# Optimization experiments

Hardware: AMD Instinct MI355X
Metric: run time of the kernel (lower is better)

The kernel has to match this reference:

```python
import jax, jax.numpy as jnp
import numpy as np

N, S, D = 8, 448, 768
VS, DS = 50000, 256
VP, DP = 200, 128
VM, DM = 400, 128
VA, DA = 360, 128
EPS_LS = 0.1
LN_EPS = 1e-12
SQRT2 = 1.4142135623730951


def setup_inputs() -> dict:
    key = jax.random.key(0)
    ks = jax.random.split(key, 20)
    total = N * S
    # all sequence lengths == S; next-token prediction uses tokens [0, S-2] as
    # inputs (hidden_sel) and tokens [1, S-1] as targets (target_sel)
    hidden_sel = np.concatenate([i * S + np.arange(S - 1) for i in range(N)]).astype(np.int32)
    target_sel = np.concatenate([i * S + np.arange(1, S) for i in range(N)]).astype(np.int32)
    tokens_lengths = (np.arange(total) % 4).astype(np.int32)  # per-token affix counts
    affix_sel = np.nonzero(tokens_lengths[target_sel] > 0)[0].astype(np.int32)

    def p(k, shape):
        return jax.random.normal(k, shape, jnp.float32) * 0.02

    inp = {
        "tr_hidden_state": jax.random.normal(ks[0], (S, N, D), jnp.float32),
        "affixes_prob": jax.random.uniform(ks[1], (total, VA), dtype=jnp.float32),
        "stems": jax.random.randint(ks[2], (total,), 0, VS, jnp.int32),
        "pos_tags": jax.random.randint(ks[3], (total,), 0, VP, jnp.int32),
        "lm_morphs": jax.random.randint(ks[4], (total,), 0, VM, jnp.int32),
        "hidden_sel_idx": jnp.asarray(hidden_sel),
        "target_sel_idx": jnp.asarray(target_sel),
        "affix_sel_idx": jnp.asarray(affix_sel),
        # stem head
        "stem_emb": p(ks[5], (VS, DS)), "stem_W": p(ks[6], (D, DS)),
        "stem_b": jnp.zeros((DS,)), "stem_g": jnp.ones((DS,)),
        "stem_beta": jnp.zeros((DS,)), "stem_bias": jnp.zeros((VS,)),
        # pos-tag head
        "pos_emb": p(ks[7], (VP, DP)), "pos_W": p(ks[8], (D, DP)),
        "pos_b": jnp.zeros((DP,)), "pos_g": jnp.ones((DP,)),
        "pos_beta": jnp.zeros((DP,)), "pos_bias": jnp.zeros((VP,)),
        # lm-morph head
        "morph_emb": p(ks[9], (VM, DM)), "morph_W": p(ks[10], (D, DM)),
        "morph_b": jnp.zeros((DM,)), "morph_g": jnp.ones((DM,)),
        "morph_beta": jnp.zeros((DM,)), "morph_bias": jnp.zeros((VM,)),
        # affixes head
        "aff_emb": p(ks[11], (VA, DA)), "aff_W": p(ks[12], (D, DA)),
        "aff_b": jnp.zeros((DA,)), "aff_g": jnp.ones((DA,)),
        "aff_beta": jnp.zeros((DA,)), "aff_bias": jnp.zeros((VA,)),
    }
    return inp


def _gelu(x):
    return x * 0.5 * (1.0 + jax.lax.erf(x / SQRT2))


def _ln(x, g, b):
    m = x.mean(-1, keepdims=True)
    v = ((x - m) ** 2).mean(-1, keepdims=True)
    return (x - m) * jax.lax.rsqrt(v + LN_EPS) * g + b


def _head(x, W, b, g, beta, emb, bias):
    h = _ln(_gelu(x @ W + b), g, beta)  # BaseHeadTransform
    return h @ emb.T + bias             # tied decoder + bias


def _ls_nll(lprobs, tgt):
    # label_smoothed_nll_loss with reduce=True, no ignore_index
    nll = -jnp.take_along_axis(lprobs, tgt[:, None], axis=1)[:, 0]
    smooth = -lprobs.sum(-1)
    nll_m, sm_m = nll.mean(), smooth.mean()
    eps_i = EPS_LS / (lprobs.shape[-1] - 1)
    return (1.0 - EPS_LS - eps_i) * nll_m + eps_i * sm_m, nll_m


def reference(tr_hidden_state, affixes_prob, stems, pos_tags, lm_morphs,
              hidden_sel_idx, target_sel_idx, affix_sel_idx,
              stem_emb, stem_W, stem_b, stem_g, stem_beta, stem_bias,
              pos_emb, pos_W, pos_b, pos_g, pos_beta, pos_bias,
              morph_emb, morph_W, morph_b, morph_g, morph_beta, morph_bias,
              aff_emb, aff_W, aff_b, aff_g, aff_beta, aff_bias):
    flat = jnp.transpose(tr_hidden_state, (1, 0, 2)).reshape(N * S, D)
    x = flat[hidden_sel_idx]  # [T, D] ragged gather of predictor states

    stem_lp = jax.nn.log_softmax(_head(x, stem_W, stem_b, stem_g, stem_beta, stem_emb, stem_bias), axis=-1)
    stem_loss, stem_nll = _ls_nll(stem_lp, stems[target_sel_idx])

    pos_lp = jax.nn.log_softmax(_head(x, pos_W, pos_b, pos_g, pos_beta, pos_emb, pos_bias), axis=-1)
    pos_loss, pos_nll = _ls_nll(pos_lp, pos_tags[target_sel_idx])

    morph_lp = jax.nn.log_softmax(_head(x, morph_W, morph_b, morph_g, morph_beta, morph_emb, morph_bias), axis=-1)
    morph_loss, morph_nll = _ls_nll(morph_lp, lm_morphs[target_sel_idx])

    xa = x[affix_sel_idx]                                # tokens with affixes
    ta = affixes_prob[target_sel_idx][affix_sel_idx]     # [Ta, VA]
    z = _head(xa, aff_W, aff_b, aff_g, aff_beta, aff_emb, aff_bias)
    aff_loss = jnp.mean(jnp.maximum(z, 0.0) - z * ta + jnp.log1p(jnp.exp(-jnp.abs(z))))

    return jnp.stack([stem_loss, pos_loss, morph_loss, aff_loss, stem_nll, pos_nll, morph_nll])
```

## Files before the change

kernel.cpp:

```cpp
#include <hip/hip_runtime.h>
#include <cstdint>
#include <cstddef>


typedef __attribute__((ext_vector_type(8))) __bf16 bf16x8;
typedef __attribute__((ext_vector_type(4))) float f32x4;
typedef __attribute__((ext_vector_type(4))) unsigned short u16x4;
typedef __attribute__((ext_vector_type(2))) unsigned short u16x2;

namespace {
constexpr int S_LEN   = 448;
constexpr int N_SEQ   = 8;
constexpr int D_MODEL = 768;
constexpr int TPAD    = 3584;
constexpr int VS = 50000, VP = 200, VM = 400, VA = 360;
constexpr int DS_STEM = 256, DS_POS = 128, DS_MORPH = 128, DS_AFF = 128;
constexpr int VS_PAD = 50176;
constexpr int VCHUNK = 32;
constexpr int VITERS = 3136 / VCHUNK;
constexpr float PAD_E = (float)(VS_PAD - VS);
constexpr int NVB_P = 1;
constexpr int NVB_M = 2;
}

__device__ __forceinline__ unsigned short f2bf(float f) {
  unsigned int u = __float_as_uint(f);
  unsigned int r = (u + 0x7FFFu + ((u >> 16) & 1u)) >> 16;
  return (unsigned short)r;
}
__device__ __forceinline__ float bf2f(unsigned short u) {
  return __uint_as_float(((unsigned int)u) << 16);
}


__global__ __launch_bounds__(256) void gather_x_kernel(
    const float* __restrict__ tr, const int* __restrict__ hsel,
    const int* __restrict__ tsel, const int* __restrict__ asel,
    const int* __restrict__ stems, const int* __restrict__ postags,
    const int* __restrict__ morphs,
    unsigned short* __restrict__ x, int* __restrict__ tgtS, int* __restrict__ tgtP,
    int* __restrict__ tgtM, int* __restrict__ arow, int T, int Ta) {
  const size_t e = (size_t)blockIdx.x * 256 + threadIdx.x;
  const int t = (int)(e / D_MODEL);
  const int d = (int)(e % D_MODEL);
  float v = 0.f;
  if (t < T) {
    int idx = hsel[t];
    int n = idx / S_LEN, s = idx % S_LEN;
    v = tr[((size_t)s * N_SEQ + n) * D_MODEL + d];
  }
  x[e] = f2bf(v);
  if (e < (size_t)T) {
    int tt = tsel[e];
    tgtS[e] = stems[tt]; tgtP[e] = postags[tt]; tgtM[e] = morphs[tt];
  }
  if (e < (size_t)Ta) arow[e] = tsel[asel[e]];
}

__global__ __launch_bounds__(256) void transpose_all_kernel(
    const float* __restrict__ sW, const float* __restrict__ pW,
    const float* __restrict__ mW, const float* __restrict__ aW,
    unsigned short* __restrict__ wtS, unsigned short* __restrict__ wtP,
    unsigned short* __restrict__ wtM, unsigned short* __restrict__ wtA) {
  const int e = blockIdx.x * 256 + threadIdx.x;
  const float* W; unsigned short* Wt; int DS; int local;
  if (e < 196608)      { W = sW; Wt = wtS; DS = 256; local = e; }
  else if (e < 294912) { W = pW; Wt = wtP; DS = 128; local = e - 196608; }
  else if (e < 393216) { W = mW; Wt = wtM; DS = 128; local = e - 294912; }
  else                 { W = aW; Wt = wtA; DS = 128; local = e - 393216; }
  const int n = local / D_MODEL, k = local % D_MODEL;
  Wt[local] = f2bf(W[(size_t)k * DS + n]);
}

__global__ __launch_bounds__(256) void conv_emb_all_kernel(
    const float* __restrict__ sE, const float* __restrict__ pE,
    const float* __restrict__ mE, const float* __restrict__ aE,
    const float* __restrict__ sb,
    unsigned short* __restrict__ dS, unsigned short* __restrict__ dP,
    unsigned short* __restrict__ dM, unsigned short* __restrict__ dA,
    float* __restrict__ bp) {
  const size_t q = ((size_t)blockIdx.x * 256 + threadIdx.x) * 4;
  if (q >= 13008896) {
    const size_t local = q - 13008896;
    float4 v = make_float4(0.f, 0.f, 0.f, 0.f);
    if (local < (size_t)VS) v = *(const float4*)(sb + local);
    *(float4*)(bp + local) = v;
    return;
  }
  const float* src; unsigned short* dst; size_t local, real;
  if (q < 12845056)            { src = sE; dst = dS; local = q;            real = 12800000; }
  else if (q < 12877824)       { src = pE; dst = dP; local = q - 12845056; real = 25600; }
  else if (q < 12943360)       { src = mE; dst = dM; local = q - 12877824; real = 51200; }
  else                         { src = aE; dst = dA; local = q - 12943360; real = 46080; }
  float4 v = make_float4(0.f, 0.f, 0.f, 0.f);
  if (local < real) v = *(const float4*)(src + local);
  u16x4 o = { f2bf(v.x), f2bf(v.y), f2bf(v.z), f2bf(v.w) };
  *(u16x4*)(dst + local) = o;
}

template <int NT>
__device__ __forceinline__ void head_body(
    const unsigned short* __restrict__ x, const unsigned short* __restrict__ Wt,
    const float* __restrict__ bvec, const float* __restrict__ gvec,
    const float* __restrict__ betav, unsigned short* __restrict__ hout) {
  constexpr int DS = NT * 16;
  const int lane = threadIdx.x & 63;
  const int wave = threadIdx.x >> 6;
  const int row0 = blockIdx.x * 32 + wave * 16;
  const int lrow = lane & 15;
  const int lk8  = (lane >> 4) * 8;

  f32x4 acc[NT];
#pragma unroll
  for (int nt = 0; nt < NT; ++nt) acc[nt] = f32x4{0.f, 0.f, 0.f, 0.f};

  const unsigned short* xrow = x + (size_t)(row0 + lrow) * D_MODEL + lk8;
#pragma unroll
  for (int ks = 0; ks < 24; ++ks) {
    bf16x8 a = *(const bf16x8*)(xrow + ks * 32);
#pragma unroll
    for (int nt = 0; nt < NT; ++nt) {
      bf16x8 b = *(const bf16x8*)(Wt + (size_t)(nt * 16 + lrow) * D_MODEL + ks * 32 + lk8);
      acc[nt] = __builtin_amdgcn_mfma_f32_16x16x32_bf16(a, b, acc[nt], 0, 0, 0);
    }
  }

  float bb[NT], gg[NT], be[NT];
#pragma unroll
  for (int nt = 0; nt < NT; ++nt) {
    int c = nt * 16 + lrow;
    bb[nt] = bvec[c]; gg[nt] = gvec[c]; be[nt] = betav[c];
  }
#pragma unroll
  for (int r = 0; r < 4; ++r) {
    const int row = row0 + (lane >> 4) * 4 + r;
    float vals[NT];
    float s = 0.f, s2 = 0.f;
#pragma unroll
    for (int nt = 0; nt < NT; ++nt) {
      float v = acc[nt][r] + bb[nt];
      v = 0.5f * v * (1.f + erff(v * 0.70710678118654752f));
      vals[nt] = v; s += v; s2 += v * v;
    }
    s  += __shfl_xor(s, 1);  s  += __shfl_xor(s, 2);  s  += __shfl_xor(s, 4);  s  += __shfl_xor(s, 8);
    s2 += __shfl_xor(s2, 1); s2 += __shfl_xor(s2, 2); s2 += __shfl_xor(s2, 4); s2 += __shfl_xor(s2, 8);
    const float mean = s * (1.f / DS);
    const float var  = s2 * (1.f / DS) - mean * mean;
    const float rstd = rsqrtf(var + 1e-12f);
#pragma unroll
    for (int nt = 0; nt < NT; ++nt) {
      float o = (vals[nt] - mean) * rstd * gg[nt] + be[nt];
      hout[(size_t)row * DS + nt * 16 + lrow] = f2bf(o);
    }
  }
}

__global__ __launch_bounds__(128, 2) void head_all_kernel(
    const unsigned short* __restrict__ x,
    const unsigned short* __restrict__ wtS, const float* __restrict__ sb,
    const float* __restrict__ sg, const float* __restrict__ sbe, unsigned short* __restrict__ hS,
    const unsigned short* __restrict__ wtP, const float* __restrict__ pb,
    const float* __restrict__ pg, const float* __restrict__ pbe, unsigned short* __restrict__ hP,
    const unsigned short* __restrict__ wtM, const float* __restrict__ mb,
    const float* __restrict__ mg, const float* __restrict__ mbe, unsigned short* __restrict__ hM,
    const unsigned short* __restrict__ wtA, const float* __restrict__ ab,
    const float* __restrict__ ag, const float* __restrict__ abe, unsigned short* __restrict__ hA) {
  if (blockIdx.y == 3)      head_body<16>(x, wtS, sb, sg, sbe, hS);
  else if (blockIdx.y == 0) head_body<8>(x, wtP, pb, pg, pbe, hP);
  else if (blockIdx.y == 1) head_body<8>(x, wtM, mb, mg, mbe, hM);
  else                      head_body<8>(x, wtA, ab, ag, abe, hA);
}


__device__ __forceinline__ void stem_role(
    const unsigned short* __restrict__ h, const unsigned short* __restrict__ emb,
    const float* __restrict__ bpad, float* __restrict__ psum,
    float* __restrict__ psum2, char* smem) {
  unsigned short (*lbuf)[4096] = (unsigned short(*)[4096])smem;
  float* lbias = (float*)(smem + 32768);

  const int f   = blockIdx.x;
  const int k2  = f >> 3;
  const int bx  = k2 % 7;
  const int by  = (k2 / 7) * 8 + (f & 7);
  const int tid  = threadIdx.x;
  const int lane = tid & 63;
  const int wave = tid >> 6;
  const int lrow = lane & 15;
  const int hi   = lane >> 4;
  const int lk8  = hi * 8;
  const int tok0 = bx * 512 + wave * 64;
  const int vbase0 = by * (VITERS * 16);

  for (int i = tid; i < VITERS * 16; i += 512) lbias[i] = bpad[vbase0 + i];

  bf16x8 hB[4][8];
#pragma unroll
  for (int tt = 0; tt < 4; ++tt)
#pragma unroll
    for (int ks = 0; ks < 8; ++ks)
      hB[tt][ks] = *(const bf16x8*)(h + (size_t)(tok0 + tt * 16 + lrow) * 256 + ks * 32 + lk8);

  const int dst16 = tid * 16;
  const int srow  = dst16 >> 9;
  const int sbyte = dst16 ^ ((srow & 7) << 4);
  const char* gs  = (const char*)emb + (size_t)vbase0 * 512 + sbyte;

  auto stage = [&](int buf, int it) {
    __builtin_amdgcn_global_load_lds(
        (const __attribute__((address_space(1))) unsigned int*)(gs + (size_t)it * 8192),
        (__attribute__((address_space(3))) unsigned int*)(&lbuf[buf][wave * 512]),
        16, 0, 0);
  };

  int loff[8];
#pragma unroll
  for (int ks = 0; ks < 8; ++ks)
    loff[ks] = (lrow * 512 + ks * 64 + hi * 16) ^ ((lrow & 7) << 4);

  float esum[4] = {0.f, 0.f, 0.f, 0.f};
  float ssum[4] = {0.f, 0.f, 0.f, 0.f};

  stage(0, 0); stage(1, 1); stage(2, 2);
  __syncthreads();

#pragma unroll 1
  for (int it = 0; it < VITERS; ++it) {
    if (it <= VITERS - 3)      asm volatile("s_waitcnt vmcnt(2)" ::: "memory");
    else if (it == VITERS - 2) asm volatile("s_waitcnt vmcnt(1)" ::: "memory");
    else                       asm volatile("s_waitcnt vmcnt(0)" ::: "memory");
    __builtin_amdgcn_s_barrier();
    if (it + 3 < VITERS) stage((it + 3) & 3, it + 3);

    const float4 bv = *(const float4*)(lbias + it * 16 + hi * 4);
    const char* lp = (const char*)(&lbuf[it & 3][0]);
    bf16x8 aA[8];
#pragma unroll
    for (int ks = 0; ks < 8; ++ks)
      aA[ks] = *(const bf16x8*)(lp + loff[ks]);

#pragma unroll
    for (int tt = 0; tt < 4; ++tt) {
      f32x4 acc = f32x4{0.f, 0.f, 0.f, 0.f};
#pragma unroll
      for (int ks = 0; ks < 8; ++ks)
        acc = __builtin_amdgcn_mfma_f32_16x16x32_bf16(aA[ks], hB[tt][ks], acc, 0, 0, 0);
      const float v0 = acc[0] + bv.x, v1 = acc[1] + bv.y;
      const float v2 = acc[2] + bv.z, v3 = acc[3] + bv.w;
      esum[tt] += (__expf(v0) + __expf(v1)) + (__expf(v2) + __expf(v3));
      ssum[tt] += (v0 + v1) + (v2 + v3);
    }
  }

#pragma unroll
  for (int tt = 0; tt < 4; ++tt) {
    float e = esum[tt], s = ssum[tt];
    e += __shfl_xor(e, 16); e += __shfl_xor(e, 32);
    s += __shfl_xor(s, 16); s += __shfl_xor(s, 32);
    if (hi == 0) {
      const int tok = tok0 + tt * 16 + lrow;
      psum [(size_t)tok * VCHUNK + by] = e;
      psum2[(size_t)tok * VCHUNK + by] = s;
    }
  }
}

__device__ __forceinline__ void pm_role(
    const unsigned short* __restrict__ h, const unsigned short* __restrict__ emb,
    const float* __restrict__ bias, float* __restrict__ psum,
    float* __restrict__ psum2, int V, int NVB, int vbx, int vby, char* smem) {
  const int t256 = threadIdx.x & 255;
  const int w8   = threadIdx.x >> 6;
  const int grp  = threadIdx.x >> 8;
  const int lane = t256 & 63;
  const int wave4 = t256 >> 6;
  const int colbase = vby * 256 + wave4 * 64;
  const int row0 = vbx * 32;
  const int lrow = lane & 15;
  const int hi   = lane >> 4;
  const int lk8  = hi * 8;
  float (*lds_e)[32] = (float(*)[32])smem;
  float (*lds_s)[32] = (float(*)[32])(smem + 1024);

  bf16x8 bfr[4][4];
  float bv[4];
  bool mk[4];
#pragma unroll
  for (int nt = 0; nt < 4; ++nt) {
    int col = colbase + nt * 16 + lrow;
#pragma unroll
    for (int ks = 0; ks < 4; ++ks)
      bfr[ks][nt] = *(const bf16x8*)(emb + (size_t)col * 128 + ks * 32 + lk8);
    mk[nt] = (col < V);
    bv[nt] = mk[nt] ? bias[col] : 0.f;
  }

  f32x4 acc[2][4];
#pragma unroll
  for (int rt = 0; rt < 2; ++rt)
#pragma unroll
    for (int nt = 0; nt < 4; ++nt) acc[rt][nt] = f32x4{0.f, 0.f, 0.f, 0.f};

  const unsigned short* hrow = h + (size_t)(row0 + lrow) * 128 + lk8;
#pragma unroll
  for (int ks = 0; ks < 4; ++ks) {
#pragma unroll
    for (int rt = 0; rt < 2; ++rt) {
      bf16x8 a = *(const bf16x8*)(hrow + (size_t)rt * 16 * 128 + ks * 32);
#pragma unroll
      for (int nt = 0; nt < 4; ++nt)
        acc[rt][nt] = __builtin_amdgcn_mfma_f32_16x16x32_bf16(a, bfr[ks][nt], acc[rt][nt], 0, 0, 0);
    }
  }

#pragma unroll
  for (int rt = 0; rt < 2; ++rt)
#pragma unroll
    for (int r = 0; r < 4; ++r) {
      float e = 0.f, s = 0.f;
#pragma unroll
      for (int nt = 0; nt < 4; ++nt) {
        float v = acc[rt][nt][r] + bv[nt];
        float ev = __expf(v);
        e += mk[nt] ? ev : 0.f;
        s += mk[nt] ? v : 0.f;
      }
      e += __shfl_xor(e, 1); e += __shfl_xor(e, 2); e += __shfl_xor(e, 4); e += __shfl_xor(e, 8);
      s += __shfl_xor(s, 1); s += __shfl_xor(s, 2); s += __shfl_xor(s, 4); s += __shfl_xor(s, 8);
      if (lrow == 0) {
        lds_e[w8][rt * 16 + hi * 4 + r] = e;
        lds_s[w8][rt * 16 + hi * 4 + r] = s;
      }
    }
  __syncthreads();
  if (t256 < 32) {
    const int rr = t256;
    const int b4 = grp * 4;
    float e = lds_e[b4][rr] + lds_e[b4 + 1][rr] + lds_e[b4 + 2][rr] + lds_e[b4 + 3][rr];
    float s = lds_s[b4][rr] + lds_s[b4 + 1][rr] + lds_s[b4 + 2][rr] + lds_s[b4 + 3][rr];
    const int row = row0 + rr;
    psum [(size_t)row * NVB + vby] = e;
    psum2[(size_t)row * NVB + vby] = s;
  }
}

__device__ __forceinline__ void aff_role(
    const unsigned short* __restrict__ h, const unsigned short* __restrict__ emb,
    const float* __restrict__ bias, const int* __restrict__ asel,
    const int* __restrict__ arow, const float* __restrict__ aprob,
    float* __restrict__ partial, int Ta, int gaff, int bx, char* smem) {
  const int t256 = threadIdx.x & 255;
  const int grp  = threadIdx.x >> 8;
  const int w8   = threadIdx.x >> 6;
  const int lane = t256 & 63;
  const int wave4 = t256 >> 6;
  const int colbase = grp * 256 + wave4 * 64;
  const int lrow = lane & 15;
  const int lk8  = (lane >> 4) * 8;
  float* wred = (float*)smem;

  bf16x8 bfr[4][4];
  float bv[4];
  bool mk[4];
#pragma unroll
  for (int nt = 0; nt < 4; ++nt) {
    int col = colbase + nt * 16 + lrow;
#pragma unroll
    for (int ks = 0; ks < 4; ++ks)
      bfr[ks][nt] = *(const bf16x8*)(emb + (size_t)col * DS_AFF + ks * 32 + lk8);
    mk[nt] = (col < VA);
    bv[nt] = mk[nt] ? bias[col] : 0.f;
  }

  float lsum = 0.f;
  {
    const int rb = bx * 16;
    const int ia = rb + lrow;
    const int srow = (ia < Ta) ? asel[ia] : 0;
    f32x4 acc[4];
#pragma unroll
    for (int nt = 0; nt < 4; ++nt) acc[nt] = f32x4{0.f, 0.f, 0.f, 0.f};
    const unsigned short* hrow = h + (size_t)srow * DS_AFF + lk8;
#pragma unroll
    for (int ks = 0; ks < 4; ++ks) {
      bf16x8 a = *(const bf16x8*)(hrow + ks * 32);
#pragma unroll
      for (int nt = 0; nt < 4; ++nt)
        acc[nt] = __builtin_amdgcn_mfma_f32_16x16x32_bf16(a, bfr[ks][nt], acc[nt], 0, 0, 0);
    }
#pragma unroll
    for (int r = 0; r < 4; ++r) {
      const int i2 = rb + (lane >> 4) * 4 + r;
      const bool live = (i2 < Ta);
      const int trow = live ? arow[i2] : 0;
#pragma unroll
      for (int nt = 0; nt < 4; ++nt) {
        if (live && mk[nt]) {
          float z = acc[nt][r] + bv[nt];
          float ta = aprob[(size_t)trow * VA + (colbase + nt * 16 + lrow)];
          lsum += fmaxf(z, 0.f) - z * ta + log1pf(__expf(-fabsf(z)));
        }
      }
    }
  }
#pragma unroll
  for (int m = 1; m < 64; m <<= 1) lsum += __shfl_xor(lsum, m);
  if (lane == 0) wred[w8] = lsum;
  __syncthreads();
  if (t256 == 0) {
    const int b4 = grp * 4;
    partial[grp * gaff + bx] = wred[b4] + wred[b4 + 1] + wred[b4 + 2] + wred[b4 + 3];
  }
}

__device__ __forceinline__ void tgt_role(
    const unsigned short* __restrict__ hS, const unsigned short* __restrict__ embS,
    const float* __restrict__ bS, const int* __restrict__ tgtS_,
    const unsigned short* __restrict__ hP, const unsigned short* __restrict__ embP,
    const float* __restrict__ bP, const int* __restrict__ tgtP_,
    const unsigned short* __restrict__ hM, const unsigned short* __restrict__ embM,
    const float* __restrict__ bM, const int* __restrict__ tgtM_,
    float* __restrict__ tlog, int T, int vb) {
  const int lane = threadIdx.x & 63;
  const int wave = threadIdx.x >> 6;
  const int t = vb * 8 + wave;
  if (t >= T) return;
  const int tg = tgtS_[t], tp = tgtP_[t], tm = tgtM_[t];
  u16x4 hv = *(const u16x4*)(hS + (size_t)t * 256 + lane * 4);
  u16x4 ev = *(const u16x4*)(embS + (size_t)tg * 256 + lane * 4);
  float d0 = bf2f(hv[0]) * bf2f(ev[0]) + bf2f(hv[1]) * bf2f(ev[1]) +
             bf2f(hv[2]) * bf2f(ev[2]) + bf2f(hv[3]) * bf2f(ev[3]);
  u16x2 hp = *(const u16x2*)(hP + (size_t)t * 128 + lane * 2);
  u16x2 ep = *(const u16x2*)(embP + (size_t)tp * 128 + lane * 2);
  float d1 = bf2f(hp[0]) * bf2f(ep[0]) + bf2f(hp[1]) * bf2f(ep[1]);
  u16x2 hm = *(const u16x2*)(hM + (size_t)t * 128 + lane * 2);
  u16x2 em = *(const u16x2*)(embM + (size_t)tm * 128 + lane * 2);
  float d2 = bf2f(hm[0]) * bf2f(em[0]) + bf2f(hm[1]) * bf2f(em[1]);
#pragma unroll
  for (int m = 1; m < 64; m <<= 1) {
    d0 += __shfl_xor(d0, m); d1 += __shfl_xor(d1, m); d2 += __shfl_xor(d2, m);
  }
  if (lane == 0) {
    tlog[t]            = d0 + bS[tg];
    tlog[TPAD + t]     = d1 + bP[tp];
    tlog[2 * TPAD + t] = d2 + bM[tm];
  }
}

__global__ __launch_bounds__(512, 2) void mega_stats_kernel(
    const unsigned short* __restrict__ hS, const unsigned short* __restrict__ embS,
    const float* __restrict__ bpadS, float* __restrict__ psS, float* __restrict__ ps2S,
    const unsigned short* __restrict__ hP, const unsigned short* __restrict__ embP,
    const float* __restrict__ p_bias, float* __restrict__ psP, float* __restrict__ ps2P,
    const unsigned short* __restrict__ hM, const unsigned short* __restrict__ embM,
    const float* __restrict__ m_bias, float* __restrict__ psM, float* __restrict__ ps2M,
    const unsigned short* __restrict__ hA, const unsigned short* __restrict__ embA,
    const float* __restrict__ a_bias, const int* __restrict__ asel,
    const int* __restrict__ arow, const float* __restrict__ aprob,
    float* __restrict__ affp,
    const float* __restrict__ s_bias, const int* __restrict__ tgtS,
    const int* __restrict__ tgtP, const int* __restrict__ tgtM,
    float* __restrict__ tlog, int T, int Ta, int gaff) {
  __shared__ alignas(16) char smem_[39040];
  const int bid = blockIdx.x;
  if (bid < 224) {
    stem_role(hS, embS, bpadS, psS, ps2S, smem_);
  } else if (bid < 280) {
    pm_role(hP, embP, p_bias, psP, ps2P, VP, NVB_P,
            (bid - 224) * 2 + (threadIdx.x >> 8), 0, smem_);
  } else if (bid < 392) {
    pm_role(hM, embM, m_bias, psM, ps2M, VM, NVB_M,
            bid - 280, threadIdx.x >> 8, smem_);
  } else if (bid < 392 + gaff) {
    aff_role(hA, embA, a_bias, asel, arow, aprob, affp, Ta, gaff, bid - 392, smem_);
  } else {
    tgt_role(hS, embS, s_bias, tgtS, hP, embP, p_bias, tgtP,
             hM, embM, m_bias, tgtM, tlog, T, bid - 392 - gaff);
  }
}

__global__ __launch_bounds__(256) void combine2_kernel(
    const float* __restrict__ psS, const float* __restrict__ ps2S,
    const float* __restrict__ psP, const float* __restrict__ ps2P,
    const float* __restrict__ psM, const float* __restrict__ ps2M,
    const float* __restrict__ tlog,
    float* __restrict__ nll, float* __restrict__ sm, int T) {
  const int lane = threadIdx.x & 63;
  const int wave = threadIdx.x >> 6;
  const int t = blockIdx.x * 4 + wave;
  if (t >= T) return;

  float z = 0.f, s = 0.f;
  if (lane < VCHUNK) {
    z = psS[(size_t)t * VCHUNK + lane];
    s = ps2S[(size_t)t * VCHUNK + lane];
  }
#pragma unroll
  for (int m = 1; m < 64; m <<= 1) { z += __shfl_xor(z, m); s += __shfl_xor(s, m); }
  if (lane == 0) {
    z -= PAD_E;
    float lz = logf(z);
    nll[t] = lz - tlog[t];
    sm[t]  = (float)VS * lz - s;

    float zP = psP[t], sP = ps2P[t];
    float lzP = logf(zP);
    nll[TPAD + t] = lzP - tlog[TPAD + t];
    sm[TPAD + t]  = (float)VP * lzP - sP;

    float zM = psM[2 * t] + psM[2 * t + 1];
    float sM = ps2M[2 * t] + ps2M[2 * t + 1];
    float lzM = logf(zM);
    nll[2 * TPAD + t] = lzM - tlog[2 * TPAD + t];
    sm[2 * TPAD + t]  = (float)VM * lzM - sM;
  }
}

__global__ __launch_bounds__(256) void finalize_kernel(
    const float* __restrict__ nll, const float* __restrict__ sm,
    const float* __restrict__ affp, int naff, float* __restrict__ out, int T, int Ta) {
  __shared__ float red[256];
  const int tid = threadIdx.x;
  float nll_m[3], sm_m[3];
  for (int h2 = 0; h2 < 3; ++h2) {
    float a = 0.f, b = 0.f;
    for (int t = tid; t < T; t += 256) { a += nll[h2 * TPAD + t]; b += sm[h2 * TPAD + t]; }
    red[tid] = a; __syncthreads();
    for (int s = 128; s > 0; s >>= 1) { if (tid < s) red[tid] += red[tid + s]; __syncthreads(); }
    float asum = red[0]; __syncthreads();
    red[tid] = b; __syncthreads();
    for (int s = 128; s > 0; s >>= 1) { if (tid < s) red[tid] += red[tid + s]; __syncthreads(); }
    float bsm = red[0]; __syncthreads();
    nll_m[h2] = asum / (float)T;
    sm_m[h2]  = bsm / (float)T;
  }
  float av = 0.f;
  for (int i = tid; i < naff; i += 256) av += affp[i];
  red[tid] = av; __syncthreads();
  for (int s = 128; s > 0; s >>= 1) { if (tid < s) red[tid] += red[tid + s]; __syncthreads(); }
  if (tid == 0) {
    const float Vv[3] = {(float)VS, (float)VP, (float)VM};
    for (int h2 = 0; h2 < 3; ++h2) {
      float eps_i = 0.1f / (Vv[h2] - 1.f);
      out[h2] = (1.0f - 0.1f - eps_i) * nll_m[h2] + eps_i * sm_m[h2];
      out[4 + h2] = nll_m[h2];
    }
    out[3] = red[0] / ((float)Ta * (float)VA);
  }
}

extern "C" void kernel_launch(void* const* d_in, const int* in_sizes, int n_in,
                              void* d_out, int out_size, void* d_ws, size_t ws_size,
                              hipStream_t stream) {
  const float* tr      = (const float*)d_in[0];
  const float* aprob   = (const float*)d_in[1];
  const int* stems     = (const int*)d_in[2];
  const int* postags   = (const int*)d_in[3];
  const int* morphs    = (const int*)d_in[4];
  const int* hsel      = (const int*)d_in[5];
  const int* tsel      = (const int*)d_in[6];
  const int* asel      = (const int*)d_in[7];
  const float* s_emb = (const float*)d_in[8],  *s_W = (const float*)d_in[9];
  const float* s_b   = (const float*)d_in[10], *s_g = (const float*)d_in[11];
  const float* s_be  = (const float*)d_in[12], *s_bias = (const float*)d_in[13];
  const float* p_emb = (const float*)d_in[14], *p_W = (const float*)d_in[15];
  const float* p_b   = (const float*)d_in[16], *p_g = (const float*)d_in[17];
  const float* p_be  = (const float*)d_in[18], *p_bias = (const float*)d_in[19];
  const float* m_emb = (const float*)d_in[20], *m_W = (const float*)d_in[21];
  const float* m_b   = (const float*)d_in[22], *m_g = (const float*)d_in[23];
  const float* m_be  = (const float*)d_in[24], *m_bias = (const float*)d_in[25];
  const float* a_emb = (const float*)d_in[26], *a_W = (const float*)d_in[27];
  const float* a_b   = (const float*)d_in[28], *a_g = (const float*)d_in[29];
  const float* a_be  = (const float*)d_in[30], *a_bias = (const float*)d_in[31];

  const int T  = in_sizes[5];
  const int Ta = in_sizes[7];

  size_t off = 0;
  auto alloc = [&](size_t nbytes) -> char* {
    char* p = (char*)d_ws + off;
    off = (off + nbytes + 255) & ~(size_t)255;
    return p;
  };
  unsigned short* x    = (unsigned short*)alloc((size_t)TPAD * D_MODEL * 2);
  unsigned short* wtS  = (unsigned short*)alloc((size_t)DS_STEM * D_MODEL * 2);
  unsigned short* wtP  = (unsigned short*)alloc((size_t)DS_POS * D_MODEL * 2);
  unsigned short* wtM  = (unsigned short*)alloc((size_t)DS_MORPH * D_MODEL * 2);
  unsigned short* wtA  = (unsigned short*)alloc((size_t)DS_AFF * D_MODEL * 2);
  unsigned short* embS = (unsigned short*)alloc((size_t)VS_PAD * DS_STEM * 2);
  unsigned short* embP = (unsigned short*)alloc((size_t)256 * DS_POS * 2);
  unsigned short* embM = (unsigned short*)alloc((size_t)512 * DS_MORPH * 2);
  unsigned short* embA = (unsigned short*)alloc((size_t)512 * DS_AFF * 2);
  unsigned short* hS   = (unsigned short*)alloc((size_t)TPAD * DS_STEM * 2);
  unsigned short* hP   = (unsigned short*)alloc((size_t)TPAD * DS_POS * 2);
  unsigned short* hM   = (unsigned short*)alloc((size_t)TPAD * DS_MORPH * 2);
  unsigned short* hA   = (unsigned short*)alloc((size_t)TPAD * DS_AFF * 2);
  float* bpadS = (float*)alloc((size_t)VS_PAD * 4);
  float* psS   = (float*)alloc((size_t)TPAD * VCHUNK * 4);
  float* ps2S  = (float*)alloc((size_t)TPAD * VCHUNK * 4);
  float* psP   = (float*)alloc((size_t)TPAD * NVB_P * 4);
  float* ps2P  = (float*)alloc((size_t)TPAD * NVB_P * 4);
  float* psM   = (float*)alloc((size_t)TPAD * NVB_M * 4);
  float* ps2M  = (float*)alloc((size_t)TPAD * NVB_M * 4);
  float* tlog  = (float*)alloc((size_t)3 * TPAD * 4);
  int*   tgtS  = (int*)alloc((size_t)TPAD * 4);
  int*   tgtP  = (int*)alloc((size_t)TPAD * 4);
  int*   tgtM  = (int*)alloc((size_t)TPAD * 4);
  int*   arow  = (int*)alloc((size_t)TPAD * 4);
  float* nllb  = (float*)alloc((size_t)3 * TPAD * 4);
  float* smb   = (float*)alloc((size_t)3 * TPAD * 4);
  float* affp  = (float*)alloc(2048);
  (void)ws_size; (void)n_in; (void)out_size;

  const int gaff = (Ta + 15) / 16;
  const int tgtb = (T + 7) / 8;

  gather_x_kernel<<<(TPAD * D_MODEL) / 256, 256, 0, stream>>>(
      tr, hsel, tsel, asel, stems, postags, morphs, x, tgtS, tgtP, tgtM, arow, T, Ta);
  transpose_all_kernel<<<491520 / 256, 256, 0, stream>>>(s_W, p_W, m_W, a_W, wtS, wtP, wtM, wtA);
  conv_emb_all_kernel<<<12753, 256, 0, stream>>>(
      s_emb, p_emb, m_emb, a_emb, s_bias, embS, embP, embM, embA, bpadS);
  head_all_kernel<<<dim3(TPAD / 32, 4), 128, 0, stream>>>(
      x, wtS, s_b, s_g, s_be, hS, wtP, p_b, p_g, p_be, hP,
      wtM, m_b, m_g, m_be, hM, wtA, a_b, a_g, a_be, hA);
  mega_stats_kernel<<<392 + gaff + tgtb, 512, 0, stream>>>(
      hS, embS, bpadS, psS, ps2S,
      hP, embP, p_bias, psP, ps2P,
      hM, embM, m_bias, psM, ps2M,
      hA, embA, a_bias, asel, arow, aprob, affp,
      s_bias, tgtS, tgtP, tgtM, tlog, T, Ta, gaff);
  combine2_kernel<<<(T + 3) / 4, 256, 0, stream>>>(psS, ps2S, psP, ps2P, psM, ps2M, tlog, nllb, smb, T);
  finalize_kernel<<<1, 256, 0, stream>>>(nllb, smb, affp, gaff * 2, (float*)d_out, T, Ta);
}
```

Baseline: 253.1 us.

## Halve mega-stats block size, fold log2e into stem embeddings, seed MFMA with bias

The fused stats kernel drops from 512 to 256 threads per block and doubles the block counts. Stem tiles now cover 256 tokens each, and the pos, morph and affix roles are rebalanced to one 256-thread group per block. The stem embeddings and bias are prescaled by log2(e) during conversion, so the inner loop can use exp2f and seed the MFMA accumulator with the bias. LN2 rescaling is applied to the stem sums and target logits afterwards. Stem LDS reads now use inline ds_read_b128 with an explicit wait and scheduling barrier. The risk is a small precision change from rounding the prescaled embeddings to bf16, plus more redundant loads of the stem embeddings across the extra blocks.

```diff
diff --git a/kernel.cpp b/kernel.cpp
--- a/kernel.cpp
+++ b/kernel.cpp
@@ -5,6 +5,7 @@
 
 typedef __attribute__((ext_vector_type(8))) __bf16 bf16x8;
 typedef __attribute__((ext_vector_type(4))) float f32x4;
+typedef __attribute__((ext_vector_type(4))) unsigned int u32x4;
 typedef __attribute__((ext_vector_type(4))) unsigned short u16x4;
 typedef __attribute__((ext_vector_type(2))) unsigned short u16x2;
 
@@ -21,6 +22,11 @@
 constexpr float PAD_E = (float)(VS_PAD - VS);
 constexpr int NVB_P = 1;
 constexpr int NVB_M = 2;
+constexpr float LOG2E = 1.4426950408889634f;
+constexpr float LN2   = 0.6931471805599453f;
+constexpr int B_STEM = 448;
+constexpr int B_P    = B_STEM + 112;
+constexpr int B_M    = B_P + 224;
 }
 
 __device__ __forceinline__ unsigned short f2bf(float f) {
@@ -84,17 +90,19 @@
     const size_t local = q - 13008896;
     float4 v = make_float4(0.f, 0.f, 0.f, 0.f);
     if (local < (size_t)VS) v = *(const float4*)(sb + local);
+    v.x *= LOG2E; v.y *= LOG2E; v.z *= LOG2E; v.w *= LOG2E;
     *(float4*)(bp + local) = v;
     return;
   }
   const float* src; unsigned short* dst; size_t local, real;
-  if (q < 12845056)            { src = sE; dst = dS; local = q;            real = 12800000; }
+  float sc = 1.f;
+  if (q < 12845056)            { src = sE; dst = dS; local = q;            real = 12800000; sc = LOG2E; }
   else if (q < 12877824)       { src = pE; dst = dP; local = q - 12845056; real = 25600; }
   else if (q < 12943360)       { src = mE; dst = dM; local = q - 12877824; real = 51200; }
   else                         { src = aE; dst = dA; local = q - 12943360; real = 46080; }
   float4 v = make_float4(0.f, 0.f, 0.f, 0.f);
   if (local < real) v = *(const float4*)(src + local);
-  u16x4 o = { f2bf(v.x), f2bf(v.y), f2bf(v.z), f2bf(v.w) };
+  u16x4 o = { f2bf(v.x * sc), f2bf(v.y * sc), f2bf(v.z * sc), f2bf(v.w * sc) };
   *(u16x4*)(dst + local) = o;
 }
 
@@ -176,23 +184,22 @@
     const unsigned short* __restrict__ h, const unsigned short* __restrict__ emb,
     const float* __restrict__ bpad, float* __restrict__ psum,
     float* __restrict__ psum2, char* smem) {
-  unsigned short (*lbuf)[4096] = (unsigned short(*)[4096])smem;
-  float* lbias = (float*)(smem + 32768);
-
-  const int f   = blockIdx.x;
-  const int k2  = f >> 3;
-  const int bx  = k2 % 7;
-  const int by  = (k2 / 7) * 8 + (f & 7);
+  const int f    = blockIdx.x;
+  const int xcd  = f & 7;
+  const int m    = f >> 3;
+  const int bx   = m % 14;
+  const int by   = (m / 14) * 8 + xcd;
   const int tid  = threadIdx.x;
   const int lane = tid & 63;
   const int wave = tid >> 6;
   const int lrow = lane & 15;
   const int hi   = lane >> 4;
   const int lk8  = hi * 8;
-  const int tok0 = bx * 512 + wave * 64;
+  const int tok0 = bx * 256 + wave * 64;
   const int vbase0 = by * (VITERS * 16);
 
-  for (int i = tid; i < VITERS * 16; i += 512) lbias[i] = bpad[vbase0 + i];
+  float* lbias = (float*)(smem + 32768);
+  for (int i = tid; i < VITERS * 16; i += 256) lbias[i] = bpad[vbase0 + i];
 
   bf16x8 hB[4][8];
 #pragma unroll
@@ -201,15 +208,21 @@
     for (int ks = 0; ks < 8; ++ks)
       hB[tt][ks] = *(const bf16x8*)(h + (size_t)(tok0 + tt * 16 + lrow) * 256 + ks * 32 + lk8);
 
-  const int dst16 = tid * 16;
-  const int srow  = dst16 >> 9;
-  const int sbyte = dst16 ^ ((srow & 7) << 4);
-  const char* gs  = (const char*)emb + (size_t)vbase0 * 512 + sbyte;
+  const int d0 = tid * 16;
+  const int s0 = d0 ^ (((d0 >> 9) & 7) << 4);
+  const char* gsA = (const char*)emb + (size_t)vbase0 * 512 + s0;
+  const char* gsB = gsA + 4096;
+
+  const unsigned ldsb = (unsigned)(size_t)(__attribute__((address_space(3))) char*)smem;
 
   auto stage = [&](int buf, int it) {
     __builtin_amdgcn_global_load_lds(
-        (const __attribute__((address_space(1))) unsigned int*)(gs + (size_t)it * 8192),
-        (__attribute__((address_space(3))) unsigned int*)(&lbuf[buf][wave * 512]),
+        (const __attribute__((address_space(1))) unsigned int*)(gsA + (size_t)it * 8192),
+        (__attribute__((address_space(3))) unsigned int*)(smem + buf * 8192 + wave * 1024),
+        16, 0, 0);
+    __builtin_amdgcn_global_load_lds(
+        (const __attribute__((address_space(1))) unsigned int*)(gsB + (size_t)it * 8192),
+        (__attribute__((address_space(3))) unsigned int*)(smem + buf * 8192 + 4096 + wave * 1024),
         16, 0, 0);
   };
 
@@ -226,29 +239,36 @@
 
 #pragma unroll 1
   for (int it = 0; it < VITERS; ++it) {
-    if (it <= VITERS - 3)      asm volatile("s_waitcnt vmcnt(2)" ::: "memory");
-    else if (it == VITERS - 2) asm volatile("s_waitcnt vmcnt(1)" ::: "memory");
+    if (it < VITERS - 2)       asm volatile("s_waitcnt vmcnt(4)" ::: "memory");
+    else if (it == VITERS - 2) asm volatile("s_waitcnt vmcnt(2)" ::: "memory");
     else                       asm volatile("s_waitcnt vmcnt(0)" ::: "memory");
     __builtin_amdgcn_s_barrier();
     if (it + 3 < VITERS) stage((it + 3) & 3, it + 3);
 
-    const float4 bv = *(const float4*)(lbias + it * 16 + hi * 4);
-    const char* lp = (const char*)(&lbuf[it & 3][0]);
+    const unsigned abuf = ldsb + (unsigned)((it & 3) * 8192);
     bf16x8 aA[8];
 #pragma unroll
-    for (int ks = 0; ks < 8; ++ks)
-      aA[ks] = *(const bf16x8*)(lp + loff[ks]);
+    for (int ks = 0; ks < 8; ++ks) {
+      u32x4 t;
+      unsigned ad = abuf + (unsigned)loff[ks];
+      asm volatile("ds_read_b128 %0, %1" : "=v"(t) : "v"(ad));
+      aA[ks] = __builtin_bit_cast(bf16x8, t);
+    }
+    u32x4 tb;
+    unsigned ab = ldsb + 32768u + (unsigned)(it * 64 + hi * 16);
+    asm volatile("ds_read_b128 %0, %1" : "=v"(tb) : "v"(ab));
+    asm volatile("s_waitcnt lgkmcnt(0)" ::: "memory");
+    __builtin_amdgcn_sched_barrier(0);
+    const f32x4 bvf = __builtin_bit_cast(f32x4, tb);
 
 #pragma unroll
     for (int tt = 0; tt < 4; ++tt) {
-      f32x4 acc = f32x4{0.f, 0.f, 0.f, 0.f};
+      f32x4 acc = bvf;
 #pragma unroll
       for (int ks = 0; ks < 8; ++ks)
         acc = __builtin_amdgcn_mfma_f32_16x16x32_bf16(aA[ks], hB[tt][ks], acc, 0, 0, 0);
-      const float v0 = acc[0] + bv.x, v1 = acc[1] + bv.y;
-      const float v2 = acc[2] + bv.z, v3 = acc[3] + bv.w;
-      esum[tt] += (__expf(v0) + __expf(v1)) + (__expf(v2) + __expf(v3));
-      ssum[tt] += (v0 + v1) + (v2 + v3);
+      esum[tt] += (exp2f(acc[0]) + exp2f(acc[1])) + (exp2f(acc[2]) + exp2f(acc[3]));
+      ssum[tt] += (acc[0] + acc[1]) + (acc[2] + acc[3]);
     }
   }
 
@@ -260,7 +280,7 @@
     if (hi == 0) {
       const int tok = tok0 + tt * 16 + lrow;
       psum [(size_t)tok * VCHUNK + by] = e;
-      psum2[(size_t)tok * VCHUNK + by] = s;
+      psum2[(size_t)tok * VCHUNK + by] = s * LN2;
     }
   }
 }
@@ -269,18 +289,16 @@
     const unsigned short* __restrict__ h, const unsigned short* __restrict__ emb,
     const float* __restrict__ bias, float* __restrict__ psum,
     float* __restrict__ psum2, int V, int NVB, int vbx, int vby, char* smem) {
-  const int t256 = threadIdx.x & 255;
-  const int w8   = threadIdx.x >> 6;
-  const int grp  = threadIdx.x >> 8;
-  const int lane = t256 & 63;
-  const int wave4 = t256 >> 6;
+  const int tid = threadIdx.x;
+  const int lane = tid & 63;
+  const int wave4 = tid >> 6;
   const int colbase = vby * 256 + wave4 * 64;
   const int row0 = vbx * 32;
   const int lrow = lane & 15;
   const int hi   = lane >> 4;
   const int lk8  = hi * 8;
   float (*lds_e)[32] = (float(*)[32])smem;
-  float (*lds_s)[32] = (float(*)[32])(smem + 1024);
+  float (*lds_s)[32] = (float(*)[32])(smem + 512);
 
   bf16x8 bfr[4][4];
   float bv[4];
@@ -328,16 +346,15 @@
       e += __shfl_xor(e, 1); e += __shfl_xor(e, 2); e += __shfl_xor(e, 4); e += __shfl_xor(e, 8);
       s += __shfl_xor(s, 1); s += __shfl_xor(s, 2); s += __shfl_xor(s, 4); s += __shfl_xor(s, 8);
       if (lrow == 0) {
-        lds_e[w8][rt * 16 + hi * 4 + r] = e;
-        lds_s[w8][rt * 16 + hi * 4 + r] = s;
+        lds_e[wave4][rt * 16 + hi * 4 + r] = e;
+        lds_s[wave4][rt * 16 + hi * 4 + r] = s;
       }
     }
   __syncthreads();
-  if (t256 < 32) {
-    const int rr = t256;
-    const int b4 = grp * 4;
-    float e = lds_e[b4][rr] + lds_e[b4 + 1][rr] + lds_e[b4 + 2][rr] + lds_e[b4 + 3][rr];
-    float s = lds_s[b4][rr] + lds_s[b4 + 1][rr] + lds_s[b4 + 2][rr] + lds_s[b4 + 3][rr];
+  if (tid < 32) {
+    const int rr = tid;
+    float e = lds_e[0][rr] + lds_e[1][rr] + lds_e[2][rr] + lds_e[3][rr];
+    float s = lds_s[0][rr] + lds_s[1][rr] + lds_s[2][rr] + lds_s[3][rr];
     const int row = row0 + rr;
     psum [(size_t)row * NVB + vby] = e;
     psum2[(size_t)row * NVB + vby] = s;
@@ -348,12 +365,10 @@
     const unsigned short* __restrict__ h, const unsigned short* __restrict__ emb,
     const float* __restrict__ bias, const int* __restrict__ asel,
     const int* __restrict__ arow, const float* __restrict__ aprob,
-    float* __restrict__ partial, int Ta, int gaff, int bx, char* smem) {
-  const int t256 = threadIdx.x & 255;
-  const int grp  = threadIdx.x >> 8;
-  const int w8   = threadIdx.x >> 6;
-  const int lane = t256 & 63;
-  const int wave4 = t256 >> 6;
+    float* __restrict__ partial, int Ta, int gaff, int bx, int grp, char* smem) {
+  const int tid = threadIdx.x;
+  const int lane = tid & 63;
+  const int wave4 = tid >> 6;
   const int colbase = grp * 256 + wave4 * 64;
   const int lrow = lane & 15;
   const int lk8  = (lane >> 4) * 8;
@@ -405,12 +420,10 @@
   }
 #pragma unroll
   for (int m = 1; m < 64; m <<= 1) lsum += __shfl_xor(lsum, m);
-  if (lane == 0) wred[w8] = lsum;
+  if (lane == 0) wred[wave4] = lsum;
   __syncthreads();
-  if (t256 == 0) {
-    const int b4 = grp * 4;
-    partial[grp * gaff + bx] = wred[b4] + wred[b4 + 1] + wred[b4 + 2] + wred[b4 + 3];
-  }
+  if (tid == 0)
+    partial[grp * gaff + bx] = wred[0] + wred[1] + wred[2] + wred[3];
 }
 
 __device__ __forceinline__ void tgt_role(
@@ -423,7 +436,7 @@
     float* __restrict__ tlog, int T, int vb) {
   const int lane = threadIdx.x & 63;
   const int wave = threadIdx.x >> 6;
-  const int t = vb * 8 + wave;
+  const int t = vb * 4 + wave;
   if (t >= T) return;
   const int tg = tgtS_[t], tp = tgtP_[t], tm = tgtM_[t];
   u16x4 hv = *(const u16x4*)(hS + (size_t)t * 256 + lane * 4);
@@ -441,13 +454,13 @@
     d0 += __shfl_xor(d0, m); d1 += __shfl_xor(d1, m); d2 += __shfl_xor(d2, m);
   }
   if (lane == 0) {
-    tlog[t]            = d0 + bS[tg];
+    tlog[t]            = d0 * LN2 + bS[tg];
     tlog[TPAD + t]     = d1 + bP[tp];
     tlog[2 * TPAD + t] = d2 + bM[tm];
   }
 }
 
-__global__ __launch_bounds__(512, 2) void mega_stats_kernel(
+__global__ __launch_bounds__(256, 2) void mega_stats_kernel(
     const unsigned short* __restrict__ hS, const unsigned short* __restrict__ embS,
     const float* __restrict__ bpadS, float* __restrict__ psS, float* __restrict__ ps2S,
     const unsigned short* __restrict__ hP, const unsigned short* __restrict__ embP,
@@ -463,19 +476,19 @@
     float* __restrict__ tlog, int T, int Ta, int gaff) {
   __shared__ alignas(16) char smem_[39040];
   const int bid = blockIdx.x;
-  if (bid < 224) {
+  if (bid < B_STEM) {
     stem_role(hS, embS, bpadS, psS, ps2S, smem_);
-  } else if (bid < 280) {
-    pm_role(hP, embP, p_bias, psP, ps2P, VP, NVB_P,
-            (bid - 224) * 2 + (threadIdx.x >> 8), 0, smem_);
-  } else if (bid < 392) {
-    pm_role(hM, embM, m_bias, psM, ps2M, VM, NVB_M,
-            bid - 280, threadIdx.x >> 8, smem_);
-  } else if (bid < 392 + gaff) {
-    aff_role(hA, embA, a_bias, asel, arow, aprob, affp, Ta, gaff, bid - 392, smem_);
+  } else if (bid < B_P) {
+    pm_role(hP, embP, p_bias, psP, ps2P, VP, NVB_P, bid - B_STEM, 0, smem_);
+  } else if (bid < B_M) {
+    const int b = bid - B_P;
+    pm_role(hM, embM, m_bias, psM, ps2M, VM, NVB_M, b >> 1, b & 1, smem_);
+  } else if (bid < B_M + 2 * gaff) {
+    const int b = bid - B_M;
+    aff_role(hA, embA, a_bias, asel, arow, aprob, affp, Ta, gaff, b >> 1, b & 1, smem_);
   } else {
     tgt_role(hS, embS, s_bias, tgtS, hP, embP, p_bias, tgtP,
-             hM, embM, m_bias, tgtM, tlog, T, bid - 392 - gaff);
+             hM, embM, m_bias, tgtM, tlog, T, bid - B_M - 2 * gaff);
   }
 }
 
@@ -613,7 +626,7 @@
   (void)ws_size; (void)n_in; (void)out_size;
 
   const int gaff = (Ta + 15) / 16;
-  const int tgtb = (T + 7) / 8;
+  const int tgtb = (T + 3) / 4;
 
   gather_x_kernel<<<(TPAD * D_MODEL) / 256, 256, 0, stream>>>(
       tr, hsel, tsel, asel, stems, postags, morphs, x, tgtS, tgtP, tgtM, arow, T, Ta);
@@ -623,7 +636,7 @@
   head_all_kernel<<<dim3(TPAD / 32, 4), 128, 0, stream>>>(
       x, wtS, s_b, s_g, s_be, hS, wtP, p_b, p_g, p_be, hP,
       wtM, m_b, m_g, m_be, hM, wtA, a_b, a_g, a_be, hA);
-  mega_stats_kernel<<<392 + gaff + tgtb, 512, 0, stream>>>(
+  mega_stats_kernel<<<B_M + 2 * gaff + tgtb, 256, 0, stream>>>(
       hS, embS, bpadS, psS, ps2S,
       hP, embP, p_bias, psP, ps2P,
       hM, embM, m_bias, psM, ps2M,
```

Result: slower. 263.0 us (+3.9%).
